# Kernel tuning notes

Hardware: AMD Instinct MI355X
Metric: run time of the kernel (lower is better)

Reference implementation:

```python
import jax, jax.numpy as jnp
import numpy as np

B, S, D, H, FF = 4, 1024, 1024, 8, 4096
DK = D // H
EPS = 1e-5


def layernorm(x, g, b):
    m = jnp.mean(x, axis=-1, keepdims=True)
    v = jnp.mean(jnp.square(x - m), axis=-1, keepdims=True)
    return (x - m) * jax.lax.rsqrt(v + EPS) * g + b


def setup_inputs() -> dict:
    key = jax.random.key(0)
    ks = jax.random.split(key, 8)
    w = lambda k, shape: jax.random.normal(k, shape, jnp.float32) * 0.02
    return {
        "x": jax.random.normal(ks[0], (B, S, D), jnp.float32),
        "mask": jnp.ones((B, 1, 1, S), jnp.int32),  # unused in 'infer' mode, kept for fidelity
        "g1": jnp.ones((D,), jnp.float32), "b1": jnp.zeros((D,), jnp.float32),
        "Wq": w(ks[1], (D, D)), "bq": jnp.zeros((D,), jnp.float32),
        "Wk": w(ks[2], (D, D)), "bk": jnp.zeros((D,), jnp.float32),
        "Wv": w(ks[3], (D, H * D)), "bv": jnp.zeros((H * D,), jnp.float32),
        "g2": jnp.ones((D,), jnp.float32), "b2": jnp.zeros((D,), jnp.float32),
        "W1": w(ks[4], (D, FF)), "bw1": jnp.zeros((FF,), jnp.float32),
        "W2": w(ks[5], (FF, D)), "bw2": jnp.zeros((D,), jnp.float32),
    }


def reference(x, mask, g1, b1, Wq, bq, Wk, bk, Wv, bv, g2, b2, W1, bw1, W2, bw2):
    # --- MultiHeadedAttention (mode='infer'; mask is ignored by this path) ---
    xn = layernorm(x, g1, b1)                                   # [B,S,D]
    q = (xn @ Wq + bq).reshape(B, S, H, DK).transpose(0, 2, 1, 3)  # [B,H,S,DK]
    k = (xn @ Wk + bk).reshape(B, S, H, DK).transpose(0, 2, 1, 3)  # [B,H,S,DK]
    v = (xn @ Wv + bv).reshape(B, S, H, D).transpose(0, 2, 1, 3)   # [B,H,S,D]
    scores = jnp.einsum('bhqd,bhkd->bhqk', q, k) / jnp.sqrt(jnp.float32(DK))
    p = jax.nn.softmax(scores, axis=-1)                          # [B,H,S,S]
    ctx = jnp.einsum('bhqk,bhkd->bhqd', p, v)                    # [B,H,S,D]
    # Source does x.view(-1, B, dim, h).sum(heads).view(B, S, dim) on the
    # contiguous [B,H,S,D] tensor: a raw row-major reshape, reproduced exactly.
    attn_out = ctx.reshape(S, B, D, H).sum(axis=-1).reshape(B, S, D)
    # --- residual + SublayerConnection (pre-norm GELU FFN) ---
    x1 = x + attn_out
    xn2 = layernorm(x1, g2, b2)
    ffn = jax.nn.gelu(xn2 @ W1 + bw1, approximate=False) @ W2 + bw2
    return x1 + ffn
```

## Files before the change

kernel.cpp:

```cpp
#include <hip/hip_runtime.h>
#include <hip/hip_bf16.h>
#include <math.h>

typedef __attribute__((ext_vector_type(8))) short   short8;
typedef __attribute__((ext_vector_type(4))) short   short4v;
typedef __attribute__((ext_vector_type(8))) __bf16  bf16x8;
typedef __attribute__((ext_vector_type(4))) float   f32x4;

typedef const __attribute__((address_space(1))) void cgv_t;
typedef __attribute__((address_space(3))) void lv_t;

__device__ __forceinline__ float bs2f(short s) {
  unsigned int u = ((unsigned int)(unsigned short)s) << 16;
  return __builtin_bit_cast(float, u);
}
__device__ __forceinline__ short f2bs(float f) {
  __hip_bfloat16 h = __float2bfloat16(f);
  return __builtin_bit_cast(short, h);
}
__device__ __forceinline__ void glds16(const short* g, short* l) {
  __builtin_amdgcn_global_load_lds((cgv_t*)g, (lv_t*)l, 16, 0, 0);
}


__global__ __launch_bounds__(256) void transpose_k(const float* __restrict__ in,
                                                   short* __restrict__ out,
                                                   int R, int C) {
  __shared__ __align__(16) short T[64 * 72];
  const int r0 = blockIdx.y * 64, c0 = blockIdx.x * 64;
  const int t = threadIdx.x;
  {
    const int rr = t >> 4;
    const int cc = (t & 15) << 2;
#pragma unroll
    for (int h = 0; h < 4; h++) {
      const int row = rr + h * 16;
      f32x4 v = *(const f32x4*)(in + (long)(r0 + row) * C + c0 + cc);
#pragma unroll
      for (int e = 0; e < 4; e++) T[row * 72 + cc + e] = f2bs(v[e]);
    }
  }
  __syncthreads();
  {
    const int cr = t >> 3;
    const int rs = (t & 7) << 3;
#pragma unroll
    for (int h = 0; h < 2; h++) {
      const int c = cr + h * 32;
      short8 v;
#pragma unroll
      for (int e = 0; e < 8; e++) v[e] = T[(rs + e) * 72 + c];
      *(short8*)(out + (long)(c0 + c) * R + r0 + rs) = v;
    }
  }
}

__global__ __launch_bounds__(256) void wv8_k(const float* __restrict__ Wv,
                                             short* __restrict__ out) {
  __shared__ __align__(16) short T[64 * 72];
  const int r0 = blockIdx.x * 64, k0 = blockIdx.y * 64;
  const int t = threadIdx.x;
  const int wave = t >> 6, lane = t & 63;
  const int r = r0 + lane;
#pragma unroll 4
  for (int i = 0; i < 16; i++) {
    const int k = k0 + wave * 16 + i;
    const float* src = Wv + (long)k * 8192 + 8 * r;
    f32x4 a = *(const f32x4*)src;
    f32x4 b = *(const f32x4*)(src + 4);
    float s = (a[0] + a[1] + a[2] + a[3]) + (b[0] + b[1] + b[2] + b[3]);
    T[lane * 72 + wave * 16 + i] = f2bs(s);
  }
  __syncthreads();
  const int rr = t >> 3, kc = (t & 7) << 3;
#pragma unroll
  for (int half = 0; half < 2; half++) {
    const int rl = rr + half * 32;
    *(short8*)(out + (long)(r0 + rl) * 1024 + k0 + kc) = *(const short8*)&T[rl * 72 + kc];
  }
}

__global__ __launch_bounds__(256) void bv8_k(const float* __restrict__ bv,
                                             float* __restrict__ out) {
  const int r = blockIdx.x * 256 + threadIdx.x;
  f32x4 a = *(const f32x4*)(bv + 8 * r);
  f32x4 b = *(const f32x4*)(bv + 8 * r + 4);
  out[r] = (a[0] + a[1] + a[2] + a[3]) + (b[0] + b[1] + b[2] + b[3]);
}

__global__ __launch_bounds__(256) void ln_k(const float* __restrict__ in,
                                            const float* __restrict__ g,
                                            const float* __restrict__ b,
                                            short* __restrict__ out) {
  const int t = threadIdx.x;
  const long base = (long)blockIdx.x * 1024 + t * 4;
  f32x4 f = *(const f32x4*)(in + base);
  float v[4] = {f[0], f[1], f[2], f[3]};
  float s1 = v[0] + v[1] + v[2] + v[3];
  float s2 = v[0]*v[0] + v[1]*v[1] + v[2]*v[2] + v[3]*v[3];
#pragma unroll
  for (int off = 32; off; off >>= 1) {
    s1 += __shfl_xor(s1, off);
    s2 += __shfl_xor(s2, off);
  }
  __shared__ float rs[4], rq[4];
  if ((t & 63) == 0) { rs[t >> 6] = s1; rq[t >> 6] = s2; }
  __syncthreads();
  s1 = rs[0] + rs[1] + rs[2] + rs[3];
  s2 = rq[0] + rq[1] + rq[2] + rq[3];
  const float mean = s1 * (1.0f / 1024.0f);
  const float var  = s2 * (1.0f / 1024.0f) - mean * mean;
  const float rstd = rsqrtf(var + 1e-5f);
  f32x4 gv = *(const f32x4*)(g + t * 4);
  f32x4 bv = *(const f32x4*)(b + t * 4);
  short4v o;
#pragma unroll
  for (int i = 0; i < 4; i++)
    o[i] = f2bs((v[i] - mean) * rstd * gv[i] + bv[i]);
  *(short4v*)(out + base) = o;
}

__global__ __launch_bounds__(256) void reduce2_k(const float* __restrict__ p0,
                                                 const float* __restrict__ p1,
                                                 const float* __restrict__ x1,
                                                 const float* __restrict__ bias,
                                                 float* __restrict__ out) {
  const int t = threadIdx.x;
  const long base = (long)blockIdx.x * 1024 + t * 4;
  f32x4 a = *(const f32x4*)(p0 + base);
  f32x4 b = *(const f32x4*)(p1 + base);
  f32x4 c = *(const f32x4*)(x1 + base);
  f32x4 d = *(const f32x4*)(bias + t * 4);
  *(f32x4*)(out + base) = a + b + c + d;
}

__global__ __launch_bounds__(256, 2) void flash_k(
    const short* __restrict__ Qg_, const short* __restrict__ Kg_,
    const short* __restrict__ V8T, const float* __restrict__ xg,
    float* __restrict__ x1) {
  __shared__ __align__(16) short smem[40960];
  short* Qs = smem;
  short* Ks = smem + 8192;
  short* Vs = smem + 24576;

  const int t = threadIdx.x;
  const int wave = t >> 6, lane = t & 63;
  const int llo = lane & 15, lhi = lane >> 4;
  const int q0 = blockIdx.x * 64;
  const int bh = blockIdx.y, b = bh >> 3, h = bh & 7;
  const float SC = 0.0883883476483184f;

  const short* Qg = Qg_ + ((long)(b * 1024 + q0)) * 1024 + h * 128;
  const short* Kg = Kg_ + ((long)b * 1024) * 1024 + h * 128;
  const short* Vg = V8T + (long)bh * 131072;

  const int srow = t >> 2, schunk = (t & 3) << 3;
  const int wbase = wave * 512;
  const int arow = (wave * 16 + llo) * 32 + lhi * 8;

#pragma unroll
  for (int kk = 0; kk < 4; kk++)
    glds16(Qg + (long)srow * 1024 + kk * 32 + schunk, Qs + kk * 2048 + wbase);

  f32x4 o[8];
  float mR[4], lR[4];
#pragma unroll
  for (int i = 0; i < 8; i++) o[i] = f32x4{0.f, 0.f, 0.f, 0.f};
#pragma unroll
  for (int r = 0; r < 4; r++) { mR[r] = -1e30f; lR[r] = 0.f; }

  for (int it = 0; it < 8; it++) {
    const int kt0 = it * 128;
#pragma unroll
    for (int kk = 0; kk < 4; kk++) {
      glds16(Kg + (long)(kt0 + srow) * 1024 + kk * 32 + schunk,
             Ks + kk * 4096 + wbase);
      glds16(Kg + (long)(kt0 + 64 + srow) * 1024 + kk * 32 + schunk,
             Ks + kk * 4096 + 2048 + wbase);
      glds16(Vg + (long)srow * 1024 + kt0 + kk * 32 + schunk,
             Vs + kk * 4096 + wbase);
      glds16(Vg + (long)(64 + srow) * 1024 + kt0 + kk * 32 + schunk,
             Vs + kk * 4096 + 2048 + wbase);
    }
    __syncthreads();

    f32x4 s[8];
#pragma unroll
    for (int i = 0; i < 8; i++) s[i] = f32x4{0.f, 0.f, 0.f, 0.f};
#pragma unroll
    for (int kk = 0; kk < 4; kk++) {
      bf16x8 aq = *(const bf16x8*)(Qs + kk * 2048 + arow);
#pragma unroll
      for (int ct = 0; ct < 8; ct++) {
        bf16x8 bk = *(const bf16x8*)(Ks + kk * 4096 + (ct * 16 + llo) * 32 + lhi * 8);
        s[ct] = __builtin_amdgcn_mfma_f32_16x16x32_bf16(aq, bk, s[ct], 0, 0, 0);
      }
    }
#pragma unroll
    for (int ct = 0; ct < 8; ct++)
#pragma unroll
      for (int r = 0; r < 4; r++) s[ct][r] *= SC;
    float alpha[4];
#pragma unroll
    for (int r = 0; r < 4; r++) {
      float mt = s[0][r];
#pragma unroll
      for (int ct = 1; ct < 8; ct++) mt = fmaxf(mt, s[ct][r]);
      mt = fmaxf(mt, __shfl_xor(mt, 1));
      mt = fmaxf(mt, __shfl_xor(mt, 2));
      mt = fmaxf(mt, __shfl_xor(mt, 4));
      mt = fmaxf(mt, __shfl_xor(mt, 8));
      const float mn = fmaxf(mR[r], mt);
      alpha[r] = expf(mR[r] - mn);
      mR[r] = mn;
    }
#pragma unroll
    for (int ct = 0; ct < 8; ct++)
#pragma unroll
      for (int r = 0; r < 4; r++) s[ct][r] = expf(s[ct][r] - mR[r]);
#pragma unroll
    for (int ct = 0; ct < 8; ct++)
#pragma unroll
      for (int r = 0; r < 4; r++) o[ct][r] *= alpha[r];
#pragma unroll
    for (int r = 0; r < 4; r++) {
      float ls = s[0][r];
#pragma unroll
      for (int ct = 1; ct < 8; ct++) ls += s[ct][r];
      ls += __shfl_xor(ls, 1);
      ls += __shfl_xor(ls, 2);
      ls += __shfl_xor(ls, 4);
      ls += __shfl_xor(ls, 8);
      lR[r] = lR[r] * alpha[r] + ls;
    }
    __syncthreads();

#pragma unroll
    for (int ct = 0; ct < 8; ct++) {
      const int base = (ct >> 1) * 4096 + ((ct & 1) << 4) + llo;
#pragma unroll
      for (int r = 0; r < 4; r++)
        Ks[base + (wave * 16 + lhi * 4 + r) * 32] = f2bs(s[ct][r]);
    }
    __syncthreads();

#pragma unroll
    for (int kk = 0; kk < 4; kk++) {
      bf16x8 ap = *(const bf16x8*)(Ks + kk * 4096 + arow);
#pragma unroll
      for (int ct = 0; ct < 8; ct++) {
        bf16x8 bv = *(const bf16x8*)(Vs + kk * 4096 + (ct * 16 + llo) * 32 + lhi * 8);
        o[ct] = __builtin_amdgcn_mfma_f32_16x16x32_bf16(ap, bv, o[ct], 0, 0, 0);
      }
    }
    __syncthreads();
  }

  float inv[4];
#pragma unroll
  for (int r = 0; r < 4; r++) inv[r] = 1.0f / lR[r];
#pragma unroll
  for (int ct = 0; ct < 8; ct++) {
#pragma unroll
    for (int r = 0; r < 4; r++) {
      const int row = q0 + wave * 16 + lhi * 4 + r;
      const long idx = ((long)(b * 8 + h) * 1024 + row) * 128 + ct * 16 + llo;
      x1[idx] = xg[idx] + o[ct][r] * inv[r];
    }
  }
}

enum { EPI_GELU = 4, EPI_QKV8 = 6, EPI_PART = 8 };

template <int EPI, int BN, int NS>
__global__ __launch_bounds__(256) void gemm128(
    const short* __restrict__ A, int lda, long azh, long azl,
    const short* __restrict__ Bt, int ldb, long bzh, long bzl,
    const float* __restrict__ bias, long biasl,
    void* __restrict__ outp, long czl, int ldc,
    const void* __restrict__ aux,
    int K) {
  constexpr int WH = (BN == 128) ? 64 : 32;
  constexpr int RT = WH / 16;
  constexpr int ASLAB = 4096;
  constexpr int BSLAB = BN * 32;
  constexpr int STAGE = NS * (ASLAB + BSLAB);
  constexpr int SMEM_SHORTS = (EPI == EPI_QKV8 && STAGE < 17408) ? 17408 : STAGE;
  __shared__ __align__(16) short smem[SMEM_SHORTS];
  short* As = smem;
  short* Bs = smem + NS * ASLAB;

  const int t = threadIdx.x;
  const int wave = t >> 6, lane = t & 63;
  const int llo = lane & 15, lhi = lane >> 4;
  const int wm = (BN == 128) ? (wave >> 1) : wave;
  const int wn = (BN == 128) ? (wave & 1) : 0;
  const int bn0 = blockIdx.x * BN, bm0 = blockIdx.y * 128;
  const int z = blockIdx.z;
  const int zh = z >> 3, zl = z & 7;

  const short* Ab = A + (long)zh * azh + (long)zl * azl;
  const short* Bb = Bt + (long)zh * bzh + (long)zl * bzl;
  bias += (long)zl * biasl;

  f32x4 acc[RT][4];
#pragma unroll
  for (int i = 0; i < RT; i++)
#pragma unroll
    for (int j = 0; j < 4; j++) acc[i][j] = f32x4{0.f, 0.f, 0.f, 0.f};

  const int srow = t >> 2, schunk = (t & 3) << 3;
  const short* Ag0 = Ab + (long)(bm0 + srow) * lda + schunk;
  const short* Ag1 = Ab + (long)(bm0 + 64 + srow) * lda + schunk;
  const short* Bg0 = Bb + (long)(bn0 + srow) * ldb + schunk;
  const short* Bg1 = Bb + (long)(bn0 + 64 + srow) * ldb + schunk;
  short* AsW0 = As + (wave * 16) * 32;
  short* AsW1 = As + (64 + wave * 16) * 32;
  short* BsW0 = Bs + (wave * 16) * 32;
  short* BsW1 = Bs + (64 + wave * 16) * 32;

  const short* aRd = As + (wm * WH + llo) * 32 + lhi * 8;
  const short* bRd = Bs + (wn * 64 + llo) * 32 + lhi * 8;

  for (int kt = 0; kt < K; kt += 32 * NS) {
#pragma unroll
    for (int s = 0; s < NS; s++) {
      glds16(Ag0 + kt + s * 32, AsW0 + s * ASLAB);
      glds16(Ag1 + kt + s * 32, AsW1 + s * ASLAB);
      glds16(Bg0 + kt + s * 32, BsW0 + s * BSLAB);
      if (BN == 128) glds16(Bg1 + kt + s * 32, BsW1 + s * BSLAB);
    }
    __syncthreads();
#pragma unroll
    for (int s = 0; s < NS; s++) {
      bf16x8 af[RT], bf[4];
#pragma unroll
      for (int i = 0; i < RT; i++)
        af[i] = *(const bf16x8*)(aRd + s * ASLAB + i * 16 * 32);
#pragma unroll
      for (int j = 0; j < 4; j++)
        bf[j] = *(const bf16x8*)(bRd + s * BSLAB + j * 16 * 32);
#pragma unroll
      for (int rt = 0; rt < RT; rt++)
#pragma unroll
        for (int ct = 0; ct < 4; ct++)
          acc[rt][ct] = __builtin_amdgcn_mfma_f32_16x16x32_bf16(af[rt], bf[ct], acc[rt][ct], 0, 0, 0);
    }
    __syncthreads();
  }

  if (EPI == EPI_GELU || (EPI == EPI_QKV8 && blockIdx.z < 2)) {
    short* C = (short*)outp + (long)z * czl;
#pragma unroll
    for (int ct = 0; ct < 4; ct++) {
      const int col = bn0 + wn * 64 + ct * 16 + llo;
      const float bval = bias[col];
#pragma unroll
      for (int rt = 0; rt < RT; rt++) {
#pragma unroll
        for (int r = 0; r < 4; r++) {
          const int row = bm0 + wm * WH + rt * 16 + lhi * 4 + r;
          float v = acc[rt][ct][r] + bval;
          if (EPI == EPI_GELU) v = 0.5f * v * (1.0f + erff(v * 0.70710678118654752f));
          C[(long)row * ldc + col] = f2bs(v);
        }
      }
    }
  } else if (EPI == EPI_QKV8) {
    short* Ts = smem;
#pragma unroll
    for (int ct = 0; ct < 4; ct++) {
      const int c = wn * 64 + ct * 16 + llo;
      const float bval = bias[bn0 + c];
#pragma unroll
      for (int rt = 0; rt < RT; rt++) {
#pragma unroll
        for (int r = 0; r < 4; r++) {
          const int row = wm * WH + rt * 16 + lhi * 4 + r;
          Ts[c * 136 + row] = f2bs(acc[rt][ct][r] + bval);
        }
      }
    }
    __syncthreads();
    const int bb = bm0 >> 10, s0 = bm0 & 1023, head = bn0 >> 7;
    short* dstbase = (short*)aux + ((long)(bb * 8 + head)) * 131072 + s0;
    const int sc8 = (t & 15) << 3;
    const int cb = t >> 4;
#pragma unroll
    for (int j = 0; j < 8; j++) {
      const int c = cb + j * 16;
      *(short8*)(dstbase + (long)c * 1024 + sc8) = *(const short8*)&Ts[c * 136 + sc8];
    }
  } else if (EPI == EPI_PART) {
    float* C = (float*)outp + (long)z * czl;
#pragma unroll
    for (int ct = 0; ct < 4; ct++) {
      const int col = bn0 + wn * 64 + ct * 16 + llo;
#pragma unroll
      for (int rt = 0; rt < RT; rt++) {
#pragma unroll
        for (int r = 0; r < 4; r++) {
          const int row = bm0 + wm * WH + rt * 16 + lhi * 4 + r;
          C[(long)row * ldc + col] = acc[rt][ct][r];
        }
      }
    }
  }
}

extern "C" void kernel_launch(void* const* d_in, const int* in_sizes, int n_in,
                              void* d_out, int out_size, void* d_ws, size_t ws_size,
                              hipStream_t stream) {
  const float* x   = (const float*)d_in[0];
  const float* g1  = (const float*)d_in[2];
  const float* b1  = (const float*)d_in[3];
  const float* Wq  = (const float*)d_in[4];
  const float* bq  = (const float*)d_in[5];
  const float* Wk  = (const float*)d_in[6];
  const float* bk  = (const float*)d_in[7];
  const float* Wv  = (const float*)d_in[8];
  const float* bv  = (const float*)d_in[9];
  const float* g2  = (const float*)d_in[10];
  const float* b2  = (const float*)d_in[11];
  const float* W1  = (const float*)d_in[12];
  const float* bw1 = (const float*)d_in[13];
  const float* W2  = (const float*)d_in[14];
  const float* bw2 = (const float*)d_in[15];

  char* ws = (char*)d_ws;
  const long MB = 1024 * 1024;
  float* bQKV = (float*)(ws);
  float* x1   = (float*)(ws + 1 * MB);
  short* wqT  = (short*)(ws + 17 * MB);
  short* wkT  = (short*)(ws + 19 * MB);
  short* wv8T = (short*)(ws + 21 * MB);
  short* xn   = (short*)(ws + 23 * MB);
  short* Q    = (short*)(ws + 31 * MB);
  short* Kb   = (short*)(ws + 39 * MB);
  short* V8T  = (short*)(ws + 47 * MB);
  short* xn2  = (short*)(ws + 17 * MB);
  short* Hb   = (short*)(ws + 25 * MB);
  short* w1T  = (short*)(ws + 57 * MB);
  short* w2T  = (short*)(ws + 65 * MB);
  float* part = (float*)(ws + 73 * MB);

  hipMemcpyAsync(bQKV, bq, 4096, hipMemcpyDeviceToDevice, stream);
  hipMemcpyAsync(bQKV + 1024, bk, 4096, hipMemcpyDeviceToDevice, stream);
  bv8_k<<<4, 256, 0, stream>>>(bv, bQKV + 2048);

  transpose_k<<<dim3(16, 16), 256, 0, stream>>>(Wq, wqT, 1024, 1024);
  transpose_k<<<dim3(16, 16), 256, 0, stream>>>(Wk, wkT, 1024, 1024);
  wv8_k<<<dim3(16, 16), 256, 0, stream>>>(Wv, wv8T);

  ln_k<<<4096, 256, 0, stream>>>(x, g1, b1, xn);

  gemm128<EPI_QKV8, 128, 2><<<dim3(8, 32, 3), 256, 0, stream>>>(
      xn, 1024, 0, 0, wqT, 1024, 0, 1048576, bQKV, 1024,
      Q, 4194304, 1024, V8T, 1024);

  flash_k<<<dim3(16, 32), 256, 0, stream>>>(Q, Kb, V8T, x, x1);

  transpose_k<<<dim3(64, 16), 256, 0, stream>>>(W1, w1T, 1024, 4096);
  transpose_k<<<dim3(16, 64), 256, 0, stream>>>(W2, w2T, 4096, 1024);

  ln_k<<<4096, 256, 0, stream>>>(x1, g2, b2, xn2);

  gemm128<EPI_GELU, 128, 2><<<dim3(32, 32, 1), 256, 0, stream>>>(
      xn2, 1024, 0, 0, w1T, 1024, 0, 0, bw1, 0,
      Hb, 0, 4096, nullptr, 1024);

  gemm128<EPI_PART, 64, 2><<<dim3(16, 32, 2), 256, 0, stream>>>(
      Hb, 4096, 0, 2048, w2T, 4096, 0, 2048, nullptr, 0,
      part, 4194304, 1024, nullptr, 2048);

  reduce2_k<<<4096, 256, 0, stream>>>(part, part + 4194304, x1, bw2,
                                      (float*)d_out);
}
```

Measured before the change: 405.5 us.

## Use 256x256-tile pipelined GEMM kernel for the FFN W1 GELU projection

Adds a dedicated 512-thread GEMM with 256x256 output tiles, double-buffered LDS staging via direct global-to-LDS loads, and explicitly interleaved phases that issue the next k-slice loads while MFMAs run. It uses s_setprio around the MFMA bursts and fuses bias plus exact GELU into the epilogue. It replaces the generic 128-tile kernel for the xn2 @ W1 step, aiming for more data reuse per tile and better load/compute overlap. The cost is 128KB of LDS and heavy register use, which limits occupancy, and only 256 blocks, which may underfill the CUs.

```diff
diff --git a/kernel.cpp b/kernel.cpp
--- a/kernel.cpp
+++ b/kernel.cpp
@@ -403,6 +403,132 @@
           const int row = bm0 + wm * WH + rt * 16 + lhi * 4 + r;
           C[(long)row * ldc + col] = acc[rt][ct][r];
         }
+      }
+    }
+  }
+}
+
+#define MF16(va, vb, vc) __builtin_amdgcn_mfma_f32_16x16x32_bf16(va, vb, vc, 0, 0, 0)
+#define FENCE asm volatile("" ::: "memory")
+#define BARRIER do { FENCE; __builtin_amdgcn_s_barrier(); FENCE; } while (0)
+#define VMW(n) asm volatile("s_waitcnt vmcnt(" #n ")" ::: "memory")
+#define NOPS ((void)0)
+
+#define STAGE_A(BUF, KH, KB) do {                                          \
+    glds16(Ag + (KB), smem + ((BUF) * 2 + (KH)) * 8192 + wofs);            \
+    glds16(Ag2 + (KB), smem + ((BUF) * 2 + (KH)) * 8192 + 4096 + wofs);    \
+  } while (0)
+#define STAGE_B(BUF, KH, KB) do {                                          \
+    glds16(Bg + (KB), smem + 32768 + ((BUF) * 2 + (KH)) * 8192 + wofs);    \
+    glds16(Bg2 + (KB), smem + 32768 + ((BUF) * 2 + (KH)) * 8192 + 4096 + wofs); \
+  } while (0)
+
+#define PHASE(RH, KH, BUF, STAGE_STMT, WAIT_STMT)                          \
+  {                                                                        \
+    const short* Ar_ = smem + ((BUF) * 2 + (KH)) * 8192 + aoff + (RH) * 2048; \
+    const short* Br_ = smem + 32768 + ((BUF) * 2 + (KH)) * 8192 + boff;    \
+    bf16x8 a0 = *(const bf16x8*)(Ar_);                                     \
+    bf16x8 a1 = *(const bf16x8*)(Ar_ + 512);                               \
+    bf16x8 a2 = *(const bf16x8*)(Ar_ + 1024);                              \
+    bf16x8 a3 = *(const bf16x8*)(Ar_ + 1536);                              \
+    bf16x8 b0 = *(const bf16x8*)(Br_);                                     \
+    bf16x8 b1 = *(const bf16x8*)(Br_ + 512);                               \
+    bf16x8 b2 = *(const bf16x8*)(Br_ + 1024);                              \
+    bf16x8 b3 = *(const bf16x8*)(Br_ + 1536);                              \
+    STAGE_STMT;                                                            \
+    BARRIER;                                                               \
+    __builtin_amdgcn_s_setprio(1);                                         \
+    acc[(RH) * 4 + 0][0] = MF16(a0, b0, acc[(RH) * 4 + 0][0]);             \
+    acc[(RH) * 4 + 0][1] = MF16(a0, b1, acc[(RH) * 4 + 0][1]);             \
+    acc[(RH) * 4 + 0][2] = MF16(a0, b2, acc[(RH) * 4 + 0][2]);             \
+    acc[(RH) * 4 + 0][3] = MF16(a0, b3, acc[(RH) * 4 + 0][3]);             \
+    acc[(RH) * 4 + 1][0] = MF16(a1, b0, acc[(RH) * 4 + 1][0]);             \
+    acc[(RH) * 4 + 1][1] = MF16(a1, b1, acc[(RH) * 4 + 1][1]);             \
+    acc[(RH) * 4 + 1][2] = MF16(a1, b2, acc[(RH) * 4 + 1][2]);             \
+    acc[(RH) * 4 + 1][3] = MF16(a1, b3, acc[(RH) * 4 + 1][3]);             \
+    acc[(RH) * 4 + 2][0] = MF16(a2, b0, acc[(RH) * 4 + 2][0]);             \
+    acc[(RH) * 4 + 2][1] = MF16(a2, b1, acc[(RH) * 4 + 2][1]);             \
+    acc[(RH) * 4 + 2][2] = MF16(a2, b2, acc[(RH) * 4 + 2][2]);             \
+    acc[(RH) * 4 + 2][3] = MF16(a2, b3, acc[(RH) * 4 + 2][3]);             \
+    acc[(RH) * 4 + 3][0] = MF16(a3, b0, acc[(RH) * 4 + 3][0]);             \
+    acc[(RH) * 4 + 3][1] = MF16(a3, b1, acc[(RH) * 4 + 3][1]);             \
+    acc[(RH) * 4 + 3][2] = MF16(a3, b2, acc[(RH) * 4 + 3][2]);             \
+    acc[(RH) * 4 + 3][3] = MF16(a3, b3, acc[(RH) * 4 + 3][3]);             \
+    __builtin_amdgcn_s_setprio(0);                                         \
+    WAIT_STMT;                                                             \
+    BARRIER;                                                               \
+  }
+
+#define TILE8(T, BUF)                                                      \
+  PHASE(0, 0, BUF, STAGE_A(1 - (BUF), 1, ((T) + 1) * 64 + 32), NOPS);      \
+  PHASE(1, 0, BUF, STAGE_B(1 - (BUF), 1, ((T) + 1) * 64 + 32), VMW(8));    \
+  PHASE(0, 1, BUF, STAGE_A(BUF, 0, ((T) + 2) * 64), NOPS);                 \
+  PHASE(1, 1, BUF, STAGE_B(BUF, 0, ((T) + 2) * 64), VMW(8))
+
+__global__ __launch_bounds__(512, 2) void gemm256_gelu(
+    const short* __restrict__ A, int lda,
+    const short* __restrict__ Bt, int ldb,
+    const float* __restrict__ bias,
+    short* __restrict__ C, int ldc, int K) {
+  __shared__ __align__(16) short smem[65536];
+
+  const int t = threadIdx.x;
+  const int wave = t >> 6, lane = t & 63;
+  const int llo = lane & 15, lhi = lane >> 4;
+  const int wm = wave >> 2, wn = wave & 3;
+  const int bm0 = blockIdx.y * 256, bn0 = blockIdx.x * 256;
+
+  const int srow = t >> 2;
+  const int sgc = (((t & 3) ^ ((t >> 3) & 3)) << 3);
+  const short* Ag  = A  + (long)(bm0 + srow) * lda + sgc;
+  const short* Ag2 = A  + (long)(bm0 + 128 + srow) * lda + sgc;
+  const short* Bg  = Bt + (long)(bn0 + srow) * ldb + sgc;
+  const short* Bg2 = Bt + (long)(bn0 + 128 + srow) * ldb + sgc;
+  const int wofs = wave * 512;
+
+  const int swz = ((lhi ^ ((llo >> 1) & 3)) << 3);
+  const int aoff = (wm * 128 + llo) * 32 + swz;
+  const int boff = (wn * 64 + llo) * 32 + swz;
+
+  f32x4 acc[8][4];
+#pragma unroll
+  for (int i = 0; i < 8; i++)
+#pragma unroll
+    for (int j = 0; j < 4; j++) acc[i][j] = f32x4{0.f, 0.f, 0.f, 0.f};
+
+  const int NT = K >> 6;
+
+  STAGE_A(0, 0, 0);  STAGE_B(0, 0, 0);
+  STAGE_A(0, 1, 32); STAGE_B(0, 1, 32);
+  STAGE_A(1, 0, 64); STAGE_B(1, 0, 64);
+  VMW(8);
+  BARRIER;
+
+  for (int tt = 0; tt < NT - 2; tt += 2) {
+    TILE8(tt, 0);
+    TILE8(tt + 1, 1);
+  }
+  PHASE(0, 0, 0, STAGE_A(1, 1, (NT - 1) * 64 + 32), NOPS);
+  PHASE(1, 0, 0, STAGE_B(1, 1, (NT - 1) * 64 + 32), VMW(8));
+  PHASE(0, 1, 0, NOPS, NOPS);
+  PHASE(1, 1, 0, NOPS, VMW(4));
+  PHASE(0, 0, 1, NOPS, NOPS);
+  PHASE(1, 0, 1, NOPS, VMW(0));
+  PHASE(0, 1, 1, NOPS, NOPS);
+  PHASE(1, 1, 1, NOPS, NOPS);
+
+#pragma unroll
+  for (int ct = 0; ct < 4; ct++) {
+    const int col = bn0 + wn * 64 + ct * 16 + llo;
+    const float bval = bias[col];
+#pragma unroll
+    for (int rt = 0; rt < 8; rt++) {
+#pragma unroll
+      for (int r = 0; r < 4; r++) {
+        const int row = bm0 + wm * 128 + rt * 16 + lhi * 4 + r;
+        float v = acc[rt][ct][r] + bval;
+        v = 0.5f * v * (1.0f + erff(v * 0.70710678118654752f));
+        C[(long)row * ldc + col] = f2bs(v);
       }
     }
   }
@@ -465,9 +591,8 @@
 
   ln_k<<<4096, 256, 0, stream>>>(x1, g2, b2, xn2);
 
-  gemm128<EPI_GELU, 128, 2><<<dim3(32, 32, 1), 256, 0, stream>>>(
-      xn2, 1024, 0, 0, w1T, 1024, 0, 0, bw1, 0,
-      Hb, 0, 4096, nullptr, 1024);
+  gemm256_gelu<<<dim3(16, 16), 512, 0, stream>>>(
+      xn2, 1024, w1T, 1024, bw1, Hb, 4096, 1024);
 
   gemm128<EPI_PART, 64, 2><<<dim3(16, 32, 2), 256, 0, stream>>>(
       Hb, 4096, 0, 2048, w2T, 4096, 0, 2048, nullptr, 0,
```

New measurement: 406.5 us. About the same (+0.3%).
